# Kernel tuning notes

Measured on AMD Instinct MI355X. Metric: run time of the kernel, lower is better.

The kernel has to match this reference:

```python
import jax, jax.numpy as jnp
import numpy as np

N_NODES = 50000
N_EDGES = 1_280_000
NODE_D = 13
EDGE_RAW_D = 1
H = 64
CONCAT_D = 2 * NODE_D + EDGE_RAW_D  # 27
NEG_SLOPE = 0.2


def _leaky(x):
    return jnp.where(x >= 0, x, NEG_SLOPE * x)


def _scatter_mean(vals, idx, num_nodes):
    # vals: [E, H]; idx: [E] int -> [num_nodes, H] mean over incident edges (0 if none)
    s = jax.ops.segment_sum(vals, idx, num_segments=num_nodes)
    cnt = jax.ops.segment_sum(jnp.ones((vals.shape[0], 1), vals.dtype), idx, num_segments=num_nodes)
    return s / jnp.maximum(cnt, 1.0)


def _conv(e, src, dst, num_nodes, w_self, b_self, w_in, w_out):
    h_self = e @ w_self + b_self
    agg_in = _scatter_mean(e, dst, num_nodes)[src]   # incoming-edge mean at src nodes
    agg_out = _scatter_mean(e, src, num_nodes)[dst]  # outgoing-edge mean at dst nodes
    return _leaky(h_self + agg_in @ w_in + agg_out @ w_out)


def setup_inputs() -> dict:
    key = jax.random.key(0)
    ks = jax.random.split(key, 24)

    def lin(k, fan_in, fan_out):
        return jax.random.normal(k, (fan_in, fan_out), jnp.float32) / np.sqrt(fan_in)

    inp = {
        'x': jax.random.normal(ks[0], (N_NODES, NODE_D), jnp.float32),
        'edge_index': jax.random.randint(ks[1], (2, N_EDGES), 0, N_NODES, jnp.int32),
        'raw_edge_attr': jax.random.normal(ks[2], (N_EDGES, EDGE_RAW_D), jnp.float32),
        'enc_w': lin(ks[3], CONCAT_D, H),
        'enc_b': jnp.zeros((H,), jnp.float32),
    }
    for i, base in zip((1, 2, 3), (4, 8, 12)):
        inp[f'w_self{i}'] = lin(ks[base], H, H)
        inp[f'b_self{i}'] = jnp.zeros((H,), jnp.float32)
        inp[f'w_in{i}'] = lin(ks[base + 1], H, H)
        inp[f'w_out{i}'] = lin(ks[base + 2], H, H)
    dims = [(H, 64), (64, 64), (64, 32), (32, 1)]
    for j, (fi, fo) in enumerate(dims, start=1):
        inp[f'mlp_w{j}'] = lin(ks[15 + j], fi, fo)
        inp[f'mlp_b{j}'] = jnp.zeros((fo,), jnp.float32)
    return inp


def reference(x, edge_index, raw_edge_attr, enc_w, enc_b,
              w_self1, b_self1, w_in1, w_out1,
              w_self2, b_self2, w_in2, w_out2,
              w_self3, b_self3, w_in3, w_out3,
              mlp_w1, mlp_b1, mlp_w2, mlp_b2, mlp_w3, mlp_b3, mlp_w4, mlp_b4):
    num_nodes = x.shape[0]
    src, dst = edge_index[0], edge_index[1]
    edge_attr = jnp.concatenate([x[src], x[dst], raw_edge_attr], axis=-1)  # [E, 27]
    h = _leaky(edge_attr @ enc_w + enc_b)
    h = _conv(h, src, dst, num_nodes, w_self1, b_self1, w_in1, w_out1)
    h = _conv(h, src, dst, num_nodes, w_self2, b_self2, w_in2, w_out2)
    h = _conv(h, src, dst, num_nodes, w_self3, b_self3, w_in3, w_out3)
    h = _leaky(h @ mlp_w1 + mlp_b1)
    h = _leaky(h @ mlp_w2 + mlp_b2)
    h = _leaky(h @ mlp_w3 + mlp_b3)
    return (h @ mlp_w4 + mlp_b4).squeeze(-1)  # [E]
```

## Files before the change

### kernel.cpp

```cpp
#include <hip/hip_runtime.h>


#define NN 50000
#define NNP 50048
#define NE 1280000
#define LDP 72
#define OFFSZ 50016
#define NB 196
#define NTILES 782
#define NPX 6250

#define WAVES 2
#define EDGE_ITERS 4
#define EDGE_BLOCKS 2500

typedef unsigned int   u32;
typedef unsigned short u16;
typedef __attribute__((ext_vector_type(8))) short  short8;
typedef __attribute__((ext_vector_type(4))) float  floatx4;

#define MFMA16(a, b, c) __builtin_amdgcn_mfma_f32_16x16x32_bf16(a, b, c, 0, 0, 0)

__device__ __forceinline__ float lrelu(float x) { return x >= 0.0f ? x : 0.2f * x; }
__device__ __forceinline__ float bf2f(u16 u) { return __uint_as_float(((u32)u) << 16); }
__device__ __forceinline__ u16 f2bf(float f) {
    u32 b = __float_as_uint(f);
    return (u16)((b + 0x7FFFu + ((b >> 16) & 1u)) >> 16);
}
__device__ __forceinline__ u32 f2bf2(float lo, float hi) {
    return (u32)f2bf(lo) | ((u32)f2bf(hi) << 16);
}

__device__ __forceinline__ short8 bfrag(const float* __restrict__ W, int ld, int n, int k0) {
    short8 b;
#pragma unroll
    for (int j = 0; j < 8; ++j) b[j] = (short)f2bf(W[(k0 + j) * ld + n]);
    return b;
}

__device__ __forceinline__ void mm_tile(const u16* __restrict__ tb,
                                        const short8 wf[2][4],
                                        floatx4 acc[4][4], int c16, int q4) {
#pragma unroll
    for (int mt = 0; mt < 4; ++mt) {
        const short8 a0 = *(const short8*)(tb + (mt * 16 + c16) * LDP + q4 * 8);
        const short8 a1 = *(const short8*)(tb + (mt * 16 + c16) * LDP + 32 + q4 * 8);
#pragma unroll
        for (int nt = 0; nt < 4; ++nt) {
            acc[mt][nt] = MFMA16(a0, wf[0][nt], acc[mt][nt]);
            acc[mt][nt] = MFMA16(a1, wf[1][nt], acc[mt][nt]);
        }
    }
}

__global__ void __launch_bounds__(256)
k_bsum(const int* __restrict__ deg_in, const int* __restrict__ deg_out,
       int* __restrict__ bsum)
{
    __shared__ int s[256];
    const int tid = threadIdx.x;
    const int i = blockIdx.x * 256 + tid;
#pragma unroll 1
    for (int pass = 0; pass < 2; ++pass) {
        const int* deg = pass ? deg_out : deg_in;
        s[tid] = (i < NN) ? deg[i] : 0;
        __syncthreads();
        for (int d = 128; d > 0; d >>= 1) {
            if (tid < d) s[tid] += s[tid + d];
            __syncthreads();
        }
        if (tid == 0) bsum[pass * NB + blockIdx.x] = s[0];
        __syncthreads();
    }
}

__global__ void __launch_bounds__(256)
k_bscan(const int* __restrict__ bsum, int* __restrict__ boff)
{
    __shared__ int s[256];
    const int tid = threadIdx.x;
#pragma unroll 1
    for (int pass = 0; pass < 2; ++pass) {
        const int v = (tid < NB) ? bsum[pass * NB + tid] : 0;
        s[tid] = v;
        __syncthreads();
        for (int d = 1; d < 256; d <<= 1) {
            const int t = (tid >= d) ? s[tid - d] : 0;
            __syncthreads();
            s[tid] += t;
            __syncthreads();
        }
        if (tid < NB) boff[pass * NB + tid] = s[tid] - v;
        __syncthreads();
    }
}

__global__ void __launch_bounds__(256)
k_bfill(const int* __restrict__ deg_in, const int* __restrict__ deg_out,
        const int* __restrict__ boff,
        int* __restrict__ off_in, int* __restrict__ off_out,
        int* __restrict__ cur_in, int* __restrict__ cur_out)
{
    __shared__ int s[256];
    const int tid = threadIdx.x;
    const int i = blockIdx.x * 256 + tid;
#pragma unroll 1
    for (int pass = 0; pass < 2; ++pass) {
        const int* deg = pass ? deg_out : deg_in;
        int* off = pass ? off_out : off_in;
        int* cur = pass ? cur_out : cur_in;
        const int v = (i < NN) ? deg[i] : 0;
        s[tid] = v;
        __syncthreads();
        for (int d = 1; d < 256; d <<= 1) {
            const int t = (tid >= d) ? s[tid - d] : 0;
            __syncthreads();
            s[tid] += t;
            __syncthreads();
        }
        const int o = boff[pass * NB + blockIdx.x] + s[tid] - v;
        if (i < NN) { off[i] = o; cur[i] = o; }
        if (i == NN - 1) off[NN] = NE;
        __syncthreads();
    }
}

__global__ void __launch_bounds__(256)
k_fill(const int* __restrict__ ei, int* __restrict__ cur_in, int* __restrict__ cur_out,
       int* __restrict__ csr_in, int* __restrict__ csr_out)
{
    const int cls   = blockIdx.x & 7;
    const int slice = blockIdx.x >> 3;
    const int base  = (slice * 256 + threadIdx.x) * 8;
    const int lo = cls * NPX, hi = lo + NPX;
    int s[8], d[8];
#pragma unroll
    for (int k = 0; k < 8; ++k) s[k] = ei[base + k];
#pragma unroll
    for (int k = 0; k < 8; ++k) d[k] = ei[NE + base + k];
#pragma unroll
    for (int k = 0; k < 8; ++k)
        if (s[k] >= lo && s[k] < hi) {
            const int p = atomicAdd(&cur_out[s[k]], 1);
            csr_out[p] = base + k;
        }
#pragma unroll
    for (int k = 0; k < 8; ++k)
        if (d[k] >= lo && d[k] < hi) {
            const int q = atomicAdd(&cur_in[d[k]], 1);
            csr_in[q] = base + k;
        }
}

__global__ void __launch_bounds__(128)
k_enc(const float* __restrict__ x, const int* __restrict__ ei,
      const float* __restrict__ raw, const float* __restrict__ wenc,
      const float* __restrict__ benc, u16* __restrict__ hm,
      int* __restrict__ deg_in, int* __restrict__ deg_out)
{
    __shared__ alignas(16) u16 tile[WAVES][64 * LDP];
    const int w = threadIdx.x >> 6, lane = threadIdx.x & 63;

    for (int it = 0; it < EDGE_ITERS; ++it) {
        const int tileId = (it * EDGE_BLOCKS + blockIdx.x) * WAVES + w;
        const int e0 = tileId * 64;

        const int ms = ei[e0 + lane];
        const int md = ei[NE + e0 + lane];
        atomicAdd(&deg_out[ms], 1);
        atomicAdd(&deg_in[md], 1);

        float f[27];
#pragma unroll
        for (int j = 0; j < 13; ++j) f[j]      = x[ms * 13 + j];
#pragma unroll
        for (int j = 0; j < 13; ++j) f[13 + j] = x[md * 13 + j];
        f[26] = raw[e0 + lane];

        float acc[64];
#pragma unroll
        for (int c = 0; c < 64; ++c) acc[c] = benc[c];
        for (int k = 0; k < 27; ++k) {
            const float vk = f[k];
#pragma unroll
            for (int c = 0; c < 64; ++c) acc[c] += vk * wenc[k * 64 + c];
        }
#pragma unroll
        for (int c = 0; c < 64; ++c) tile[w][lane * LDP + c] = f2bf(lrelu(acc[c]));
        for (int i = 0; i < 64; ++i)
            hm[(size_t)(e0 + i) * 64 + lane] = tile[w][i * LDP + lane];
    }
}

__global__ void __launch_bounds__(256)
k_mean(const u16* __restrict__ hm,
       const int* __restrict__ off_in, const int* __restrict__ csr_in,
       const int* __restrict__ off_out, const int* __restrict__ csr_out,
       u16* __restrict__ m_in, u16* __restrict__ m_out)
{
    const int w = threadIdx.x >> 6, lane = threadIdx.x & 63;
    const int node = blockIdx.x * 4 + w;
    const int rg = lane >> 3;
    const int co = (lane & 7) * 8;

    for (int pass = 0; pass < 2; ++pass) {
        const int* off = pass ? off_out : off_in;
        const int* csr = pass ? csr_out : csr_in;
        u16* mp        = pass ? m_out : m_in;

        const int b0 = off[node], b1 = off[node + 1];
        float fa[8], fb[8];
#pragma unroll
        for (int c = 0; c < 8; ++c) { fa[c] = 0.f; fb[c] = 0.f; }

        int j = b0;
        for (; j + 16 <= b1; j += 16) {
            const int ea = csr[j + rg];
            const int eb = csr[j + 8 + rg];
            const short8 va = *(const short8*)(hm + (size_t)ea * 64 + co);
            const short8 vb = *(const short8*)(hm + (size_t)eb * 64 + co);
#pragma unroll
            for (int c = 0; c < 8; ++c) fa[c] += bf2f((u16)va[c]);
#pragma unroll
            for (int c = 0; c < 8; ++c) fb[c] += bf2f((u16)vb[c]);
        }
        for (; j < b1; j += 8) {
            const int jj = j + rg;
            const int idx = jj < b1 ? jj : b0;
            const float fl = jj < b1 ? 1.f : 0.f;
            const int e = csr[idx];
            const short8 v = *(const short8*)(hm + (size_t)e * 64 + co);
#pragma unroll
            for (int c = 0; c < 8; ++c) fa[c] += fl * bf2f((u16)v[c]);
        }
#pragma unroll
        for (int c = 0; c < 8; ++c) fa[c] += fb[c];
#pragma unroll
        for (int d = 8; d < 64; d <<= 1)
#pragma unroll
            for (int c = 0; c < 8; ++c) fa[c] += __shfl_xor(fa[c], d, 64);

        const int deg = b1 - b0;
        const float inv = 1.0f / (float)(deg > 0 ? deg : 1);
        if (lane < 8) {
            uint4 p;
            p.x = f2bf2(fa[0] * inv, fa[1] * inv);
            p.y = f2bf2(fa[2] * inv, fa[3] * inv);
            p.z = f2bf2(fa[4] * inv, fa[5] * inv);
            p.w = f2bf2(fa[6] * inv, fa[7] * inv);
            *(uint4*)(mp + (size_t)node * 64 + lane * 8) = p;
        }
    }
}

__global__ void __launch_bounds__(256)
k_nodemm(const u16* __restrict__ m_in, const u16* __restrict__ m_out,
         const float* __restrict__ w_in, const float* __restrict__ w_out,
         u16* __restrict__ t_in, u16* __restrict__ t_out)
{
    const int w = threadIdx.x >> 6, lane = threadIdx.x & 63;
    const int c16 = lane & 15, q4 = lane >> 4;
    const int tileId = blockIdx.x * 4 + w;
    if (tileId >= NTILES) return;
    const int n0 = tileId * 64;

    for (int pass = 0; pass < 2; ++pass) {
        const u16* mp   = pass ? m_out : m_in;
        const float* wp = pass ? w_out : w_in;
        u16* tp         = pass ? t_out : t_in;

        short8 wf[2][4];
#pragma unroll
        for (int ks = 0; ks < 2; ++ks)
#pragma unroll
            for (int nt = 0; nt < 4; ++nt)
                wf[ks][nt] = bfrag(wp, 64, nt * 16 + c16, ks * 32 + q4 * 8);

#pragma unroll
        for (int mt = 0; mt < 4; ++mt) {
            const short8* ap = (const short8*)(mp + (size_t)(n0 + mt * 16 + c16) * 64 + q4 * 8);
            const short8 a0 = ap[0];
            const short8 a1 = ap[4];
            floatx4 acc[4];
#pragma unroll
            for (int nt = 0; nt < 4; ++nt) acc[nt] = (floatx4)(0.0f);
#pragma unroll
            for (int nt = 0; nt < 4; ++nt) {
                acc[nt] = MFMA16(a0, wf[0][nt], acc[nt]);
                acc[nt] = MFMA16(a1, wf[1][nt], acc[nt]);
            }
#pragma unroll
            for (int nt = 0; nt < 4; ++nt)
#pragma unroll
                for (int r = 0; r < 4; ++r) {
                    const int node = n0 + mt * 16 + q4 * 4 + r;
                    if (node < NN)
                        tp[(size_t)node * 64 + nt * 16 + c16] = f2bf(acc[nt][r]);
                }
        }
    }
}

__global__ void __launch_bounds__(128, 4)
k_edge(const float* __restrict__ wself, const float* __restrict__ bself,
       const u16* __restrict__ t_in, const u16* __restrict__ t_out,
       const int* __restrict__ ei, u16* __restrict__ hm)
{
    __shared__ int sidx[WAVES][64], didx[WAVES][64];
    const int w = threadIdx.x >> 6, lane = threadIdx.x & 63;
    const int c16 = lane & 15, q4 = lane >> 4;

    short8 wf[2][4];
    float bias[4];
#pragma unroll
    for (int ks = 0; ks < 2; ++ks)
#pragma unroll
        for (int nt = 0; nt < 4; ++nt)
            wf[ks][nt] = bfrag(wself, 64, nt * 16 + c16, ks * 32 + q4 * 8);
#pragma unroll
    for (int nt = 0; nt < 4; ++nt) bias[nt] = bself[nt * 16 + c16];

    for (int it = 0; it < EDGE_ITERS; ++it) {
        const int tileId = (it * EDGE_BLOCKS + blockIdx.x) * WAVES + w;
        const int e0 = tileId * 64;
        sidx[w][lane] = ei[e0 + lane];
        didx[w][lane] = ei[NE + e0 + lane];

#pragma unroll
        for (int mt = 0; mt < 4; ++mt) {
            const short8* ap = (const short8*)(hm + (size_t)(e0 + mt * 16 + c16) * 64 + q4 * 8);
            const short8 a0 = ap[0];
            const short8 a1 = ap[4];
            floatx4 acc[4];
#pragma unroll
            for (int nt = 0; nt < 4; ++nt) acc[nt] = (floatx4)(0.0f);
#pragma unroll
            for (int nt = 0; nt < 4; ++nt) {
                acc[nt] = MFMA16(a0, wf[0][nt], acc[nt]);
                acc[nt] = MFMA16(a1, wf[1][nt], acc[nt]);
            }
            float tv[4][4], uv[4][4];
#pragma unroll
            for (int r = 0; r < 4; ++r) {
                const int s = sidx[w][mt * 16 + q4 * 4 + r];
#pragma unroll
                for (int nt = 0; nt < 4; ++nt)
                    tv[r][nt] = bf2f(t_in[(size_t)s * 64 + nt * 16 + c16]);
            }
#pragma unroll
            for (int r = 0; r < 4; ++r) {
                const int d = didx[w][mt * 16 + q4 * 4 + r];
#pragma unroll
                for (int nt = 0; nt < 4; ++nt)
                    uv[r][nt] = bf2f(t_out[(size_t)d * 64 + nt * 16 + c16]);
            }
#pragma unroll
            for (int nt = 0; nt < 4; ++nt)
#pragma unroll
                for (int r = 0; r < 4; ++r) {
                    const int row = mt * 16 + q4 * 4 + r;
                    const float v = acc[nt][r] + bias[nt] + tv[r][nt] + uv[r][nt];
                    hm[(size_t)(e0 + row) * 64 + nt * 16 + c16] = f2bf(lrelu(v));
                }
        }
    }
}

__global__ void __launch_bounds__(128, 2)
k_edge_mlp(const float* __restrict__ wself, const float* __restrict__ bself,
           const u16* __restrict__ t_in, const u16* __restrict__ t_out,
           const int* __restrict__ ei, const u16* __restrict__ hm,
           const float* __restrict__ w1, const float* __restrict__ b1,
           const float* __restrict__ w2, const float* __restrict__ b2,
           const float* __restrict__ w3, const float* __restrict__ b3,
           const float* __restrict__ w4, const float* __restrict__ b4,
           float* __restrict__ out)
{
    __shared__ alignas(16) u16 tile[WAVES][64 * LDP];
    __shared__ int sidx[WAVES][64], didx[WAVES][64];
    const int w = threadIdx.x >> 6, lane = threadIdx.x & 63;
    const int c16 = lane & 15, q4 = lane >> 4;

    short8 wfS[2][4], wf1[2][4], wf2[2][4], wf3[2][2];
    float bS[4], bv1[4], bv2[4], bv3[2];
#pragma unroll
    for (int ks = 0; ks < 2; ++ks) {
#pragma unroll
        for (int nt = 0; nt < 4; ++nt) {
            wfS[ks][nt] = bfrag(wself, 64, nt * 16 + c16, ks * 32 + q4 * 8);
            wf1[ks][nt] = bfrag(w1,    64, nt * 16 + c16, ks * 32 + q4 * 8);
            wf2[ks][nt] = bfrag(w2,    64, nt * 16 + c16, ks * 32 + q4 * 8);
        }
#pragma unroll
        for (int nt = 0; nt < 2; ++nt)
            wf3[ks][nt] = bfrag(w3, 32, nt * 16 + c16, ks * 32 + q4 * 8);
    }
#pragma unroll
    for (int nt = 0; nt < 4; ++nt) { bS[nt] = bself[nt*16+c16]; bv1[nt] = b1[nt*16+c16]; bv2[nt] = b2[nt*16+c16]; }
#pragma unroll
    for (int nt = 0; nt < 2; ++nt) bv3[nt] = b3[nt * 16 + c16];
    const float w4a = w4[c16], w4b = w4[16 + c16], b4v = b4[0];

    for (int it = 0; it < EDGE_ITERS; ++it) {
        const int tileId = (it * EDGE_BLOCKS + blockIdx.x) * WAVES + w;
        const int e0 = tileId * 64;
        sidx[w][lane] = ei[e0 + lane];
        didx[w][lane] = ei[NE + e0 + lane];

#pragma unroll
        for (int mt = 0; mt < 4; ++mt) {
            const short8* ap = (const short8*)(hm + (size_t)(e0 + mt * 16 + c16) * 64 + q4 * 8);
            const short8 a0 = ap[0];
            const short8 a1 = ap[4];
            floatx4 acc[4];
#pragma unroll
            for (int nt = 0; nt < 4; ++nt) acc[nt] = (floatx4)(0.0f);
#pragma unroll
            for (int nt = 0; nt < 4; ++nt) {
                acc[nt] = MFMA16(a0, wfS[0][nt], acc[nt]);
                acc[nt] = MFMA16(a1, wfS[1][nt], acc[nt]);
            }
            float tv[4][4], uv[4][4];
#pragma unroll
            for (int r = 0; r < 4; ++r) {
                const int s = sidx[w][mt * 16 + q4 * 4 + r];
#pragma unroll
                for (int nt = 0; nt < 4; ++nt)
                    tv[r][nt] = bf2f(t_in[(size_t)s * 64 + nt * 16 + c16]);
            }
#pragma unroll
            for (int r = 0; r < 4; ++r) {
                const int d = didx[w][mt * 16 + q4 * 4 + r];
#pragma unroll
                for (int nt = 0; nt < 4; ++nt)
                    uv[r][nt] = bf2f(t_out[(size_t)d * 64 + nt * 16 + c16]);
            }
#pragma unroll
            for (int nt = 0; nt < 4; ++nt)
#pragma unroll
                for (int r = 0; r < 4; ++r) {
                    const int row = mt * 16 + q4 * 4 + r;
                    const float v = acc[nt][r] + bS[nt] + tv[r][nt] + uv[r][nt];
                    tile[w][row * LDP + nt * 16 + c16] = f2bf(lrelu(v));
                }
        }

        floatx4 acc[4][4];
#pragma unroll
        for (int mt = 0; mt < 4; ++mt)
#pragma unroll
            for (int nt = 0; nt < 4; ++nt) acc[mt][nt] = (floatx4)(0.0f);
        mm_tile(tile[w], wf1, acc, c16, q4);
#pragma unroll
        for (int mt = 0; mt < 4; ++mt)
#pragma unroll
            for (int nt = 0; nt < 4; ++nt)
#pragma unroll
                for (int r = 0; r < 4; ++r)
                    tile[w][(mt * 16 + q4 * 4 + r) * LDP + nt * 16 + c16] =
                        f2bf(lrelu(acc[mt][nt][r] + bv1[nt]));

#pragma unroll
        for (int mt = 0; mt < 4; ++mt)
#pragma unroll
            for (int nt = 0; nt < 4; ++nt) acc[mt][nt] = (floatx4)(0.0f);
        mm_tile(tile[w], wf2, acc, c16, q4);
#pragma unroll
        for (int mt = 0; mt < 4; ++mt)
#pragma unroll
            for (int nt = 0; nt < 4; ++nt)
#pragma unroll
                for (int r = 0; r < 4; ++r)
                    tile[w][(mt * 16 + q4 * 4 + r) * LDP + nt * 16 + c16] =
                        f2bf(lrelu(acc[mt][nt][r] + bv2[nt]));

        floatx4 a3[4][2];
#pragma unroll
        for (int mt = 0; mt < 4; ++mt)
#pragma unroll
            for (int nt = 0; nt < 2; ++nt) a3[mt][nt] = (floatx4)(0.0f);
#pragma unroll
        for (int mt = 0; mt < 4; ++mt) {
            const short8 a0 = *(const short8*)(tile[w] + (mt * 16 + c16) * LDP + q4 * 8);
            const short8 a1 = *(const short8*)(tile[w] + (mt * 16 + c16) * LDP + 32 + q4 * 8);
#pragma unroll
            for (int nt = 0; nt < 2; ++nt) {
                a3[mt][nt] = MFMA16(a0, wf3[0][nt], a3[mt][nt]);
                a3[mt][nt] = MFMA16(a1, wf3[1][nt], a3[mt][nt]);
            }
        }
#pragma unroll
        for (int mt = 0; mt < 4; ++mt)
#pragma unroll
            for (int r = 0; r < 4; ++r) {
                float p = lrelu(a3[mt][0][r] + bv3[0]) * w4a
                        + lrelu(a3[mt][1][r] + bv3[1]) * w4b;
                p += __shfl_xor(p, 1, 64);
                p += __shfl_xor(p, 2, 64);
                p += __shfl_xor(p, 4, 64);
                p += __shfl_xor(p, 8, 64);
                if (c16 == 0) out[e0 + mt * 16 + q4 * 4 + r] = p + b4v;
            }
    }
}

extern "C" void kernel_launch(void* const* d_in, const int* in_sizes, int n_in,
                              void* d_out, int out_size, void* d_ws, size_t ws_size,
                              hipStream_t stream)
{
    const float* x      = (const float*)d_in[0];
    const int*   ei     = (const int*)  d_in[1];
    const float* raw    = (const float*)d_in[2];
    const float* wenc   = (const float*)d_in[3];
    const float* benc   = (const float*)d_in[4];
    const float* wself1 = (const float*)d_in[5];
    const float* bself1 = (const float*)d_in[6];
    const float* win1   = (const float*)d_in[7];
    const float* wout1  = (const float*)d_in[8];
    const float* wself2 = (const float*)d_in[9];
    const float* bself2 = (const float*)d_in[10];
    const float* win2   = (const float*)d_in[11];
    const float* wout2  = (const float*)d_in[12];
    const float* wself3 = (const float*)d_in[13];
    const float* bself3 = (const float*)d_in[14];
    const float* win3   = (const float*)d_in[15];
    const float* wout3  = (const float*)d_in[16];
    const float* w1 = (const float*)d_in[17]; const float* b1 = (const float*)d_in[18];
    const float* w2 = (const float*)d_in[19]; const float* b2 = (const float*)d_in[20];
    const float* w3 = (const float*)d_in[21]; const float* b3 = (const float*)d_in[22];
    const float* w4 = (const float*)d_in[23]; const float* b4 = (const float*)d_in[24];

    u16*   t_in    = (u16*)d_ws;
    u16*   t_out   = t_in + (size_t)NN * 64;
    int*   deg_in  = (int*)(t_out + (size_t)NN * 64);
    int*   deg_out = deg_in + NN;
    int*   cur_in  = deg_out + NN;
    int*   cur_out = cur_in + NN;
    int*   off_in  = cur_out + NN;
    int*   off_out = off_in + OFFSZ;
    int*   csr_in  = off_out + OFFSZ;
    int*   csr_out = csr_in + NE;
    int*   bsum    = csr_out + NE;
    int*   boff    = bsum + 512;
    u16*   m_in    = (u16*)(boff + 512);
    u16*   m_out   = m_in + (size_t)NNP * 64;
    u16*   hm      = m_out + (size_t)NNP * 64;

    hipMemsetAsync(deg_in, 0, (size_t)2 * NN * sizeof(int), stream);

    k_enc<<<EDGE_BLOCKS, 128, 0, stream>>>(x, ei, raw, wenc, benc, hm, deg_in, deg_out);

    k_bsum <<<NB, 256, 0, stream>>>(deg_in, deg_out, bsum);
    k_bscan<<<1,  256, 0, stream>>>(bsum, boff);
    k_bfill<<<NB, 256, 0, stream>>>(deg_in, deg_out, boff, off_in, off_out, cur_in, cur_out);
    k_fill<<<8 * (NE / 2048), 256, 0, stream>>>(ei, cur_in, cur_out, csr_in, csr_out);

    for (int layer = 0; layer < 3; ++layer) {
        const float* wi = layer == 0 ? win1  : layer == 1 ? win2  : win3;
        const float* wo = layer == 0 ? wout1 : layer == 1 ? wout2 : wout3;
        k_mean<<<NN / 4, 256, 0, stream>>>(hm, off_in, csr_in, off_out, csr_out,
                                           m_in, m_out);
        k_nodemm<<<NB, 256, 0, stream>>>(m_in, m_out, wi, wo, t_in, t_out);
        if (layer == 0)
            k_edge<<<EDGE_BLOCKS, 128, 0, stream>>>(wself1, bself1, t_in, t_out, ei, hm);
        else if (layer == 1)
            k_edge<<<EDGE_BLOCKS, 128, 0, stream>>>(wself2, bself2, t_in, t_out, ei, hm);
        else
            k_edge_mlp<<<EDGE_BLOCKS, 128, 0, stream>>>(wself3, bself3, t_in, t_out, ei, hm,
                                                        w1, b1, w2, b2, w3, b3, w4, b4,
                                                        (float*)d_out);
    }
}
```

Baseline: 901.2 us.

## Move encoder matmul to bf16 MFMA and split degree counting into partitioned kernel

The edge encoder's scalar 27x64 FMA loop is replaced by bf16 MFMA. Inputs are staged as a zero-padded 32-wide bf16 row in LDS, and the weights are held in registers as MFMA fragments. Degree counting moves out of the encoder into a separate k_deg kernel that bins atomics by node range, like the existing fill kernel, to improve atomic locality. The cost is an extra launch, a second read of edge_index, and bf16 rounding of the encoder inputs. hm is now written with 2-byte scattered stores straight from MFMA output rather than through the LDS transpose.

```diff
diff --git a/kernel.cpp b/kernel.cpp
--- a/kernel.cpp
+++ b/kernel.cpp
@@ -51,6 +51,26 @@
             acc[mt][nt] = MFMA16(a1, wf[1][nt], acc[mt][nt]);
         }
     }
+}
+
+__global__ void __launch_bounds__(256)
+k_deg(const int* __restrict__ ei, int* __restrict__ deg_in, int* __restrict__ deg_out)
+{
+    const int cls   = blockIdx.x & 7;
+    const int slice = blockIdx.x >> 3;
+    const int base  = (slice * 256 + threadIdx.x) * 8;
+    const int lo = cls * NPX, hi = lo + NPX;
+    int s[8], d[8];
+#pragma unroll
+    for (int k = 0; k < 8; ++k) s[k] = ei[base + k];
+#pragma unroll
+    for (int k = 0; k < 8; ++k) d[k] = ei[NE + base + k];
+#pragma unroll
+    for (int k = 0; k < 8; ++k)
+        if (s[k] >= lo && s[k] < hi) atomicAdd(&deg_out[s[k]], 1);
+#pragma unroll
+    for (int k = 0; k < 8; ++k)
+        if (d[k] >= lo && d[k] < hi) atomicAdd(&deg_in[d[k]], 1);
 }
 
 __global__ void __launch_bounds__(256)
@@ -155,11 +175,25 @@
 __global__ void __launch_bounds__(128)
 k_enc(const float* __restrict__ x, const int* __restrict__ ei,
       const float* __restrict__ raw, const float* __restrict__ wenc,
-      const float* __restrict__ benc, u16* __restrict__ hm,
-      int* __restrict__ deg_in, int* __restrict__ deg_out)
+      const float* __restrict__ benc, u16* __restrict__ hm)
 {
     __shared__ alignas(16) u16 tile[WAVES][64 * LDP];
     const int w = threadIdx.x >> 6, lane = threadIdx.x & 63;
+    const int c16 = lane & 15, q4 = lane >> 4;
+
+    short8 wf[4];
+    float bias[4];
+#pragma unroll
+    for (int nt = 0; nt < 4; ++nt) {
+        short8 b;
+#pragma unroll
+        for (int j = 0; j < 8; ++j) {
+            const int k = q4 * 8 + j;
+            b[j] = (short)(k < 27 ? f2bf(wenc[k * 64 + nt * 16 + c16]) : 0);
+        }
+        wf[nt] = b;
+        bias[nt] = benc[nt * 16 + c16];
+    }
 
     for (int it = 0; it < EDGE_ITERS; ++it) {
         const int tileId = (it * EDGE_BLOCKS + blockIdx.x) * WAVES + w;
@@ -167,28 +201,33 @@
 
         const int ms = ei[e0 + lane];
         const int md = ei[NE + e0 + lane];
-        atomicAdd(&deg_out[ms], 1);
-        atomicAdd(&deg_in[md], 1);
-
-        float f[27];
-#pragma unroll
-        for (int j = 0; j < 13; ++j) f[j]      = x[ms * 13 + j];
-#pragma unroll
-        for (int j = 0; j < 13; ++j) f[13 + j] = x[md * 13 + j];
-        f[26] = raw[e0 + lane];
-
-        float acc[64];
-#pragma unroll
-        for (int c = 0; c < 64; ++c) acc[c] = benc[c];
-        for (int k = 0; k < 27; ++k) {
-            const float vk = f[k];
-#pragma unroll
-            for (int c = 0; c < 64; ++c) acc[c] += vk * wenc[k * 64 + c];
-        }
-#pragma unroll
-        for (int c = 0; c < 64; ++c) tile[w][lane * LDP + c] = f2bf(lrelu(acc[c]));
-        for (int i = 0; i < 64; ++i)
-            hm[(size_t)(e0 + i) * 64 + lane] = tile[w][i * LDP + lane];
+
+        u16* row = tile[w] + lane * LDP;
+#pragma unroll
+        for (int j = 0; j < 13; ++j) row[j]      = f2bf(x[ms * 13 + j]);
+#pragma unroll
+        for (int j = 0; j < 13; ++j) row[13 + j] = f2bf(x[md * 13 + j]);
+        row[26] = f2bf(raw[e0 + lane]);
+#pragma unroll
+        for (int j = 27; j < 32; ++j) row[j] = 0;
+
+#pragma unroll
+        for (int mt = 0; mt < 4; ++mt) {
+            const short8 a = *(const short8*)(tile[w] + (mt * 16 + c16) * LDP + q4 * 8);
+            floatx4 acc[4];
+#pragma unroll
+            for (int nt = 0; nt < 4; ++nt) acc[nt] = (floatx4)(0.0f);
+#pragma unroll
+            for (int nt = 0; nt < 4; ++nt) acc[nt] = MFMA16(a, wf[nt], acc[nt]);
+#pragma unroll
+            for (int nt = 0; nt < 4; ++nt)
+#pragma unroll
+                for (int r = 0; r < 4; ++r) {
+                    const int rowi = mt * 16 + q4 * 4 + r;
+                    hm[(size_t)(e0 + rowi) * 64 + nt * 16 + c16] =
+                        f2bf(lrelu(acc[nt][r] + bias[nt]));
+                }
+        }
     }
 }
 
@@ -548,7 +587,9 @@
 
     hipMemsetAsync(deg_in, 0, (size_t)2 * NN * sizeof(int), stream);
 
-    k_enc<<<EDGE_BLOCKS, 128, 0, stream>>>(x, ei, raw, wenc, benc, hm, deg_in, deg_out);
+    k_deg<<<8 * (NE / 2048), 256, 0, stream>>>(ei, deg_in, deg_out);
+
+    k_enc<<<EDGE_BLOCKS, 128, 0, stream>>>(x, ei, raw, wenc, benc, hm);
 
     k_bsum <<<NB, 256, 0, stream>>>(deg_in, deg_out, bsum);
     k_bscan<<<1,  256, 0, stream>>>(bsum, boff);
```

After: 955.4 us. 1.06x slower.
